# Kernel optimization log

Measured on AMD Instinct MI355X. Metric: run time of the kernel, lower is better.

Reference implementation:

```python
import jax, jax.numpy as jnp
import numpy as np

N = 16384   # total gate nodes (64 graphs x 256 gates)
B = 64      # graphs in batch
E = 49152   # directed edges (avg in-degree 3)
Q = 32      # qubit_num
F = 256     # feat_dim
D = 2 * F   # node feature dim = 512
H = 2       # heads
A = 128     # action_num


def _gatv2(x, wl, wr, att, b, src, dst, n):
    # PyG GATv2Conv (concat=True, share_weights=False, negative_slope=0.2)
    h, c = att.shape
    xl = (x @ wl).reshape(n, h, c)   # source-side projection [N,H,C]
    xr = (x @ wr).reshape(n, h, c)   # target-side projection [N,H,C]
    e = jax.nn.leaky_relu(xl[src] + xr[dst], 0.2)       # [E,H,C]
    logit = jnp.einsum('ehc,hc->eh', e, att)             # [E,H]
    m = jax.ops.segment_max(logit, dst, num_segments=n)  # softmax over in-edges per target
    p = jnp.exp(logit - m[dst])
    den = jax.ops.segment_sum(p, dst, num_segments=n)
    alpha = p / den[dst]                                 # [E,H]
    out = jax.ops.segment_sum(alpha[:, :, None] * xl[src], dst, num_segments=n)
    return out.reshape(n, h * c) + b


def _forward(x, xt_w1, xt_b1, xt_w2, xt_b2,
             g0_wl, g0_wr, g0_att, g0_b,
             g1_wl, g1_wr, g1_att, g1_b,
             g2_wl, g2_wr, g2_att, g2_b,
             g3_wl, g3_wr, g3_att, g3_b,
             g4_wl, g4_wr, g4_att, g4_b,
             ln_w, ln_b, aggr_t,
             m_w1, m_b1, m_w2, m_b2, m_w3, m_b3,
             edge_index, batch):
    lr = lambda v: jax.nn.leaky_relu(v, 0.01)
    # x_trans: Linear -> LeakyReLU -> Linear, then fold qubit-pairs into one node
    h0 = lr(x @ xt_w1 + xt_b1) @ xt_w2 + xt_b2           # [2N, F]
    cx = h0.reshape(-1, D)                               # [N, 2F]
    n = cx.shape[0]
    # GATv2Conv default add_self_loops=True (inputs contain no self loops)
    sl = jnp.arange(n, dtype=edge_index.dtype)
    src = jnp.concatenate([edge_index[0], sl])
    dst = jnp.concatenate([edge_index[1], sl])
    res = cx
    h = lr(_gatv2(cx, g0_wl, g0_wr, g0_att, g0_b, src, dst, n))
    for wl_, wr_, att_, b_ in ((g1_wl, g1_wr, g1_att, g1_b),
                               (g2_wl, g2_wr, g2_att, g2_b),
                               (g3_wl, g3_wr, g3_att, g3_b)):
        h = lr(_gatv2(h, wl_, wr_, att_, b_, src, dst, n))
    h = lr(_gatv2(h, g4_wl, g4_wr, g4_att, g4_b, src, dst, n))
    h = h + res                                           # residual [N, 2F]
    # PyG LayerNorm(mode='graph'): normalize over nodes AND channels per graph
    cnt = jax.ops.segment_sum(jnp.ones((n,), h.dtype), batch, num_segments=B)
    norm = cnt * h.shape[1]
    mean = jax.ops.segment_sum(h.sum(-1), batch, num_segments=B) / norm
    hc = h - mean[batch][:, None]
    var = jax.ops.segment_sum((hc * hc).sum(-1), batch, num_segments=B) / norm
    h = hc / jnp.sqrt(var + 1e-5)[batch][:, None] * ln_w + ln_b
    # SoftmaxAggregation(learn=True): channel-wise softmax over nodes per graph
    logit = h * aggr_t
    mg = jax.ops.segment_max(logit, batch, num_segments=B)
    p = jnp.exp(logit - mg[batch])
    den = jax.ops.segment_sum(p, batch, num_segments=B)
    g = jax.ops.segment_sum((p / den[batch]) * h, batch, num_segments=B)  # [B, 2F]
    # head MLP 512->384->256->128
    o = lr(g @ m_w1 + m_b1)
    o = lr(o @ m_w2 + m_b2)
    return o @ m_w3 + m_b3


def setup_inputs() -> dict:
    key = jax.random.key(0)
    ks = iter(jax.random.split(key, 64))
    def rn(shp, s=0.05):
        return jax.random.normal(next(ks), shp, jnp.float32) * s
    d = {}
    d['x'] = jax.random.normal(next(ks), (2 * N, Q), jnp.float32)
    src = jax.random.randint(next(ks), (E,), 0, N, jnp.int32)
    off = jax.random.randint(next(ks), (E,), 1, N, jnp.int32)
    d['edge_index'] = jnp.stack([src, (src + off) % N])  # no self loops
    d['batch'] = jnp.arange(N, dtype=jnp.int32) // (N // B)
    d['xt_w1'] = rn((Q, F)); d['xt_b1'] = rn((F,))
    d['xt_w2'] = rn((F, F)); d['xt_b2'] = rn((F,))
    d['g0_wl'] = rn((D, H * D)); d['g0_wr'] = rn((D, H * D))
    d['g0_att'] = rn((H, D));    d['g0_b'] = rn((H * D,))
    for i in (1, 2, 3):
        d[f'g{i}_wl'] = rn((H * D, H * D)); d[f'g{i}_wr'] = rn((H * D, H * D))
        d[f'g{i}_att'] = rn((H, D));        d[f'g{i}_b'] = rn((H * D,))
    d['g4_wl'] = rn((H * D, D)); d['g4_wr'] = rn((H * D, D))
    d['g4_att'] = rn((1, D));    d['g4_b'] = rn((D,))
    d['ln_w'] = jnp.ones((D,), jnp.float32); d['ln_b'] = jnp.zeros((D,), jnp.float32)
    d['aggr_t'] = jnp.array(1.0, jnp.float32)
    d['m_w1'] = rn((D, 384)); d['m_b1'] = rn((384,))
    d['m_w2'] = rn((384, 256)); d['m_b2'] = rn((256,))
    d['m_w3'] = rn((256, A)); d['m_b3'] = rn((A,))
    return d


def reference(x, edge_index, batch, xt_w1, xt_b1, xt_w2, xt_b2,
              g0_wl, g0_wr, g0_att, g0_b,
              g1_wl, g1_wr, g1_att, g1_b,
              g2_wl, g2_wr, g2_att, g2_b,
              g3_wl, g3_wr, g3_att, g3_b,
              g4_wl, g4_wr, g4_att, g4_b,
              ln_w, ln_b, aggr_t,
              m_w1, m_b1, m_w2, m_b2, m_w3, m_b3):
    return _forward(x, xt_w1, xt_b1, xt_w2, xt_b2,
                    g0_wl, g0_wr, g0_att, g0_b,
                    g1_wl, g1_wr, g1_att, g1_b,
                    g2_wl, g2_wr, g2_att, g2_b,
                    g3_wl, g3_wr, g3_att, g3_b,
                    g4_wl, g4_wr, g4_att, g4_b,
                    ln_w, ln_b, aggr_t,
                    m_w1, m_b1, m_w2, m_b2, m_w3, m_b3,
                    edge_index, batch)
```

## Files before the change

kernel.cpp:

```cpp
#include <hip/hip_runtime.h>
#include <hip/hip_bf16.h>

typedef __hip_bfloat16 bf16;

#define NN 16384
#define BBG 64
#define EE 49152
#define ET (EE + NN)
#define DD 512
#define NG (NN / BBG)

__device__ __forceinline__ float b2f(bf16 v) { return __bfloat162float(v); }
__device__ __forceinline__ bf16 f2b(float v) { return __float2bfloat16(v); }
__device__ __forceinline__ float sb2f(short s) {
    unsigned u = ((unsigned)(unsigned short)s) << 16;
    return __builtin_bit_cast(float, u);
}
__device__ __forceinline__ short f2bs(float v) {
    bf16 b = f2b(v);
    return __builtin_bit_cast(short, b);
}
__device__ __forceinline__ int clampi(int v, int lo, int hi)
{
    return v < lo ? lo : (v > hi ? hi : v);
}

typedef __attribute__((ext_vector_type(8))) short bf16x8;
typedef __attribute__((ext_vector_type(4))) float f32x4;

#define AS1 __attribute__((address_space(1)))
#define AS3 __attribute__((address_space(3)))

__global__ __launch_bounds__(256) void gemm_mfma_bt(
    const bf16* __restrict__ A, const bf16* __restrict__ Bt,
    const float* __restrict__ bias, float* __restrict__ C,
    bf16* __restrict__ Cb, int M, int N, int K, float slope, int has_act)
{
    __shared__ bf16 As[128 * 32];
    __shared__ bf16 Bs[128 * 32];
    const int tid = threadIdx.x;
    const int w = tid >> 6;
    const int l = tid & 63;
    const int bm = blockIdx.y * 128;
    const int bn = blockIdx.x * 128;
    const int wrow = (w >> 1) * 64;
    const int wcol = (w & 1) * 64;
    const int quad = l >> 4;
    const int c16 = l & 15;

    const int lrow = l >> 2;
    const int lchunk = l & 3;
    const bf16* Ag = A + (size_t)(bm + w * 16 + lrow) * K + lchunk * 8;
    const bf16* Bg = Bt + (size_t)(bn + w * 16 + lrow) * K + lchunk * 8;
    char* AsB = (char*)As;
    char* BsB = (char*)Bs;

    f32x4 acc[4][4] = {};

    for (int k0 = 0; k0 < K; k0 += 32) {
        __builtin_amdgcn_global_load_lds((const AS1 void*)(Ag + k0),
            (AS3 void*)(AsB + w * 1024), 16, 0, 0);
        __builtin_amdgcn_global_load_lds((const AS1 void*)(Ag + (size_t)64 * K + k0),
            (AS3 void*)(AsB + 4096 + w * 1024), 16, 0, 0);
        __builtin_amdgcn_global_load_lds((const AS1 void*)(Bg + k0),
            (AS3 void*)(BsB + w * 1024), 16, 0, 0);
        __builtin_amdgcn_global_load_lds((const AS1 void*)(Bg + (size_t)64 * K + k0),
            (AS3 void*)(BsB + 4096 + w * 1024), 16, 0, 0);
        __syncthreads();

        bf16x8 a[4], b[4];
#pragma unroll
        for (int i = 0; i < 4; i++) {
            int ra = wrow + i * 16 + c16;
            a[i] = *(const bf16x8*)(AsB + ra * 64 + quad * 16);
            int rb = wcol + i * 16 + c16;
            b[i] = *(const bf16x8*)(BsB + rb * 64 + quad * 16);
        }
#pragma unroll
        for (int i = 0; i < 4; i++)
#pragma unroll
            for (int j = 0; j < 4; j++)
                acc[i][j] = __builtin_amdgcn_mfma_f32_16x16x32_bf16(
                    a[i], b[j], acc[i][j], 0, 0, 0);
        __syncthreads();
    }

#pragma unroll
    for (int i = 0; i < 4; i++) {
#pragma unroll
        for (int j = 0; j < 4; j++) {
            int col = bn + wcol + j * 16 + c16;
            float bv = bias ? bias[col] : 0.f;
#pragma unroll
            for (int r = 0; r < 4; r++) {
                int row = bm + wrow + i * 16 + quad * 4 + r;
                float v = acc[i][j][r] + bv;
                if (has_act) v = (v >= 0.f) ? v : v * slope;
                if (C)  C[(size_t)row * N + col] = v;
                if (Cb) Cb[(size_t)row * N + col] = f2b(v);
            }
        }
    }
}

__global__ __launch_bounds__(256) void gemm_mfma_dual(
    const bf16* __restrict__ A, const bf16* __restrict__ Bt,
    bf16* __restrict__ X0, bf16* __restrict__ X1,
    int M, int Ntot, int K, int HC)
{
    __shared__ bf16 As[128 * 32];
    __shared__ bf16 Bs[128 * 32];
    const int tid = threadIdx.x;
    const int w = tid >> 6;
    const int l = tid & 63;
    const int bm = blockIdx.y * 128;
    const int bn = blockIdx.x * 128;
    const int wrow = (w >> 1) * 64;
    const int wcol = (w & 1) * 64;
    const int quad = l >> 4;
    const int c16 = l & 15;

    const int lrow = l >> 2;
    const int lchunk = l & 3;
    const bf16* Ag = A + (size_t)(bm + w * 16 + lrow) * K + lchunk * 8;
    const bf16* Bg = Bt + (size_t)(bn + w * 16 + lrow) * K + lchunk * 8;
    char* AsB = (char*)As;
    char* BsB = (char*)Bs;

    f32x4 acc[4][4] = {};

    for (int k0 = 0; k0 < K; k0 += 32) {
        __builtin_amdgcn_global_load_lds((const AS1 void*)(Ag + k0),
            (AS3 void*)(AsB + w * 1024), 16, 0, 0);
        __builtin_amdgcn_global_load_lds((const AS1 void*)(Ag + (size_t)64 * K + k0),
            (AS3 void*)(AsB + 4096 + w * 1024), 16, 0, 0);
        __builtin_amdgcn_global_load_lds((const AS1 void*)(Bg + k0),
            (AS3 void*)(BsB + w * 1024), 16, 0, 0);
        __builtin_amdgcn_global_load_lds((const AS1 void*)(Bg + (size_t)64 * K + k0),
            (AS3 void*)(BsB + 4096 + w * 1024), 16, 0, 0);
        __syncthreads();

        bf16x8 a[4], b[4];
#pragma unroll
        for (int i = 0; i < 4; i++) {
            int ra = wrow + i * 16 + c16;
            a[i] = *(const bf16x8*)(AsB + ra * 64 + quad * 16);
            int rb = wcol + i * 16 + c16;
            b[i] = *(const bf16x8*)(BsB + rb * 64 + quad * 16);
        }
#pragma unroll
        for (int i = 0; i < 4; i++)
#pragma unroll
            for (int j = 0; j < 4; j++)
                acc[i][j] = __builtin_amdgcn_mfma_f32_16x16x32_bf16(
                    a[i], b[j], acc[i][j], 0, 0, 0);
        __syncthreads();
    }

#pragma unroll
    for (int i = 0; i < 4; i++) {
#pragma unroll
        for (int j = 0; j < 4; j++) {
            int col = bn + wcol + j * 16 + c16;
            bf16* dst = (col < HC) ? (X0 + col) : (X1 + col - HC);
#pragma unroll
            for (int r = 0; r < 4; r++) {
                int row = bm + wrow + i * 16 + quad * 4 + r;
                dst[(size_t)row * HC] = f2b(acc[i][j][r]);
            }
        }
    }
}

__global__ __launch_bounds__(256) void gemm_f32(
    const float* __restrict__ A, const float* __restrict__ W,
    const float* __restrict__ bias, float* __restrict__ C,
    int M, int N, int K, float slope, int has_act)
{
    const int BK = 16;
    __shared__ float Asm[BK][64 + 1];
    __shared__ float Wsm[BK][64 + 1];
    int tid = threadIdx.x;
    int bm = blockIdx.y * 64;
    int bn = blockIdx.x * 64;
    int tr = tid >> 4;
    int tc = tid & 15;
    float acc[4][4] = {};

    for (int k0 = 0; k0 < K; k0 += BK) {
        {
            int col = tid & 15;
            int row = tid >> 4;
#pragma unroll
            for (int p = 0; p < 4; p++) {
                int r = row + p * 16;
                Asm[col][r] = A[(size_t)(bm + r) * K + k0 + col];
            }
        }
        {
            int wc = tid & 63;
            int wr = tid >> 6;
#pragma unroll
            for (int p = 0; p < 4; p++) {
                int r = wr + p * 4;
                Wsm[r][wc] = W[(size_t)(k0 + r) * N + bn + wc];
            }
        }
        __syncthreads();
#pragma unroll
        for (int kk = 0; kk < BK; kk++) {
            float a[4], w[4];
#pragma unroll
            for (int i = 0; i < 4; i++) a[i] = Asm[kk][tr * 4 + i];
#pragma unroll
            for (int j = 0; j < 4; j++) w[j] = Wsm[kk][tc * 4 + j];
#pragma unroll
            for (int i = 0; i < 4; i++)
#pragma unroll
                for (int j = 0; j < 4; j++)
                    acc[i][j] += a[i] * w[j];
        }
        __syncthreads();
    }
#pragma unroll
    for (int i = 0; i < 4; i++) {
        int r = bm + tr * 4 + i;
#pragma unroll
        for (int j = 0; j < 4; j++) {
            int cn = bn + tc * 4 + j;
            float v = acc[i][j];
            if (bias) v += bias[cn];
            if (has_act) v = (v >= 0.f) ? v : v * slope;
            C[(size_t)r * N + cn] = v;
        }
    }
}

__global__ __launch_bounds__(256) void transpose_f2b2(
    const float* __restrict__ in0, bf16* __restrict__ out0,
    const float* __restrict__ in1, bf16* __restrict__ out1, int R, int C)
{
    const float* in = blockIdx.z ? in1 : in0;
    bf16* out = blockIdx.z ? out1 : out0;
    __shared__ float tile[32][33];
    int c0 = blockIdx.x * 32;
    int r0 = blockIdx.y * 32;
    int tx = threadIdx.x & 31;
    int ty = threadIdx.x >> 5;
#pragma unroll
    for (int k = 0; k < 4; k++) {
        int r = ty + k * 8;
        tile[r][tx] = in[(size_t)(r0 + r) * C + c0 + tx];
    }
    __syncthreads();
#pragma unroll
    for (int k = 0; k < 4; k++) {
        int rr = ty + k * 8;
        out[(size_t)(c0 + rr) * R + r0 + tx] = f2b(tile[tx][rr]);
    }
}

__global__ void f2b_vec(const float* __restrict__ in, bf16* __restrict__ out, int n)
{
    int i = blockIdx.x * 256 + threadIdx.x;
    if (i < n) out[i] = f2b(in[i]);
}

__global__ void count_deg(const int* __restrict__ ei, int* __restrict__ deg)
{
    int e = blockIdx.x * 256 + threadIdx.x;
    if (e >= ET) return;
    int d = (e < EE) ? ei[EE + e] : (e - EE);
    d = clampi(d, 0, NN - 1);
    atomicAdd(&deg[d], 1);
}

__global__ __launch_bounds__(256) void scan_deg(const int* __restrict__ deg,
                                                int* __restrict__ rs)
{
    __shared__ int part[256];
    __shared__ int psum[257];
    int tid = threadIdx.x;
    const int per = NN / 256;
    int base = tid * per;
    int s = 0;
    for (int i = 0; i < per; i++) s += deg[base + i];
    part[tid] = s;
    __syncthreads();
    if (tid == 0) {
        int acc = 0;
        for (int i = 0; i < 256; i++) { psum[i] = acc; acc += part[i]; }
        psum[256] = acc;
    }
    __syncthreads();
    int acc = psum[tid];
    for (int i = 0; i < per; i++) { rs[base + i] = acc; acc += deg[base + i]; }
    if (tid == 0) rs[NN] = psum[256];
}

__global__ void fill_csr(const int* __restrict__ ei, const int* __restrict__ rs,
                         int* __restrict__ cur, int* __restrict__ csrc)
{
    int e = blockIdx.x * 256 + threadIdx.x;
    if (e >= ET) return;
    int s, d;
    if (e < EE) { s = ei[e]; d = ei[EE + e]; } else { s = d = e - EE; }
    s = clampi(s, 0, NN - 1);
    d = clampi(d, 0, NN - 1);
    int pos = atomicAdd(&cur[d], 1);
    int slot = clampi(rs[d] + pos, 0, ET - 1);
    csrc[slot] = s;
}

template<int NH>
__global__ __launch_bounds__(256, 4) void gat_wave5(
    const bf16* __restrict__ xl, const bf16* __restrict__ xr,
    const float* __restrict__ att, const float* __restrict__ bias,
    const int* __restrict__ rs, const int* __restrict__ csrc,
    const float* __restrict__ res, float* __restrict__ out_f,
    bf16* __restrict__ out_b, float* __restrict__ lnsums)
{
    constexpr int HC = NH * 512;
    constexpr int PF = 6;
    constexpr int NODES = (NH == 2) ? 8 : 4;
    const int tid = threadIdx.x;
    const int w = tid >> 6;
    const int lane = tid & 63;
    const int wave_id = blockIdx.x * 4 + w;

    int msrc[NODES];
    int sdeg[NODES];
#pragma unroll
    for (int it = 0; it < NODES; ++it) {
        int gw = wave_id * NODES + it;
        int n = (NH == 2) ? (gw >> 1) : gw;
        int st = rs[n];
        int deg = clampi(rs[n + 1] - st, 1, 64);
        st = clampi(st, 0, ET - 1);
        st = __builtin_amdgcn_readfirstlane(st);
        deg = __builtin_amdgcn_readfirstlane(deg);
        sdeg[it] = deg;
        msrc[it] = csrc[st + ((lane < deg) ? lane : deg - 1)];
    }
    if (NH == 2) {
        asm volatile("" : "+v"(msrc[0]), "+v"(msrc[1]), "+v"(msrc[2]),
                          "+v"(msrc[3]), "+v"(msrc[4]), "+v"(msrc[5]),
                          "+v"(msrc[6]), "+v"(msrc[7]));
    } else {
        asm volatile("" : "+v"(msrc[0]), "+v"(msrc[1]), "+v"(msrc[2]),
                          "+v"(msrc[3]));
    }

    float av0[8], av1[8];
    {
        f32x4 t0 = *(const f32x4*)(att + lane * 8);
        f32x4 t1 = *(const f32x4*)(att + lane * 8 + 4);
#pragma unroll
        for (int k = 0; k < 4; k++) { av0[k] = t0[k]; av0[4 + k] = t1[k]; }
        if (NH == 2) {
            f32x4 t2 = *(const f32x4*)(att + 512 + lane * 8);
            f32x4 t3 = *(const f32x4*)(att + 512 + lane * 8 + 4);
#pragma unroll
            for (int k = 0; k < 4; k++) { av1[k] = t2[k]; av1[4 + k] = t3[k]; }
        } else {
#pragma unroll
            for (int k = 0; k < 8; k++) av1[k] = av0[k];
        }
    }

    f32x4 rows[2][PF];
    f32x4 rpx[2];

    auto issue = [&](int it, int pb) {
        int gw = wave_id * NODES + it;
        int n = (NH == 2) ? (gw >> 1) : gw;
        int h = (NH == 2) ? (gw & 1) : 0;
        int cb = h * 512 + lane * 8;
        rpx[pb] = *(const f32x4*)(xr + (size_t)n * HC + cb);
        int dm1 = sdeg[it] - 1;
#pragma unroll
        for (int r = 0; r < PF; r++) {
            int idx = (r < dm1) ? r : dm1;
            int s = __builtin_amdgcn_readlane(msrc[it], idx);
            s = clampi(s, 0, NN - 1);
            rows[pb][r] = *(const f32x4*)(xl + (size_t)s * HC + cb);
        }
    };
    auto pin = [&](int pb) {
        asm volatile("" : "+v"(rows[pb][0]), "+v"(rows[pb][1]),
                          "+v"(rows[pb][2]), "+v"(rows[pb][3]),
                          "+v"(rows[pb][4]), "+v"(rows[pb][5]), "+v"(rpx[pb]));
    };

    auto compute = [&](int it, int pb) {
        int gw = wave_id * NODES + it;
        int n = (NH == 2) ? (gw >> 1) : gw;
        int h = (NH == 2) ? (gw & 1) : 0;
        int cb = h * 512 + lane * 8;
        int deg = sdeg[it];

        float rv[8], av[8];
        {
            bf16x8 xb = __builtin_bit_cast(bf16x8, rpx[pb]);
#pragma unroll
            for (int k = 0; k < 8; k++) {
                rv[k] = sb2f(xb[k]);
                av[k] = h ? av1[k] : av0[k];
            }
        }

        float part[PF];
#pragma unroll
        for (int r = 0; r < PF; r++) {
            bf16x8 rb = __builtin_bit_cast(bf16x8, rows[pb][r]);
            float p0 = 0.f, p1 = 0.f, p2 = 0.f, p3 = 0.f;
#pragma unroll
            for (int k = 0; k < 8; k += 4) {
                float x0 = sb2f(rb[k + 0]);
                float x1 = sb2f(rb[k + 1]);
                float x2 = sb2f(rb[k + 2]);
                float x3 = sb2f(rb[k + 3]);
                float u0 = x0 + rv[k + 0]; u0 = (u0 >= 0.f) ? u0 : 0.2f * u0;
                float u1 = x1 + rv[k + 1]; u1 = (u1 >= 0.f) ? u1 : 0.2f * u1;
                float u2 = x2 + rv[k + 2]; u2 = (u2 >= 0.f) ? u2 : 0.2f * u2;
                float u3 = x3 + rv[k + 3]; u3 = (u3 >= 0.f) ? u3 : 0.2f * u3;
                p0 = fmaf(av[k + 0], u0, p0);
                p1 = fmaf(av[k + 1], u1, p1);
                p2 = fmaf(av[k + 2], u2, p2);
                p3 = fmaf(av[k + 3], u3, p3);
            }
            part[r] = (p0 + p1) + (p2 + p3);
        }

#pragma unroll
        for (int msk = 32; msk; msk >>= 1) {
#pragma unroll
            for (int r = 0; r < PF; r++) part[r] += __shfl_xor(part[r], msk);
        }

        float m = -1e30f;
#pragma unroll
        for (int r = 0; r < PF; r++) {
            float vr = (r < deg) ? part[r] : -1e30f;
            m = fmaxf(m, vr);
        }
        float den = 0.f;
        float pw[PF];
#pragma unroll
        for (int r = 0; r < PF; r++) {
            float e = __expf(part[r] - m);
            pw[r] = (r < deg) ? e : 0.f;
            den += pw[r];
        }

        float acc[8];
#pragma unroll
        for (int k = 0; k < 8; k++) acc[k] = 0.f;
#pragma unroll
        for (int r = 0; r < PF; r++) {
            bf16x8 rb = __builtin_bit_cast(bf16x8, rows[pb][r]);
#pragma unroll
            for (int k = 0; k < 8; k++)
                acc[k] = fmaf(pw[r], sb2f(rb[k]), acc[k]);
        }

        if (deg > PF) {
            for (int i = PF; i < deg; i++) {
                int s = __builtin_amdgcn_readlane(msrc[it], i);
                s = clampi(s, 0, NN - 1);
                f32x4 rw = *(const f32x4*)(xl + (size_t)s * HC + cb);
                bf16x8 rb = __builtin_bit_cast(bf16x8, rw);
                float pt = 0.f;
#pragma unroll
                for (int k = 0; k < 8; k++) {
                    float x = sb2f(rb[k]);
                    float u = x + rv[k];
                    u = (u >= 0.f) ? u : 0.2f * u;
                    pt = fmaf(av[k], u, pt);
                }
#pragma unroll
                for (int msk = 32; msk; msk >>= 1) pt += __shfl_xor(pt, msk);
                float mn = fmaxf(m, pt);
                float rr = __expf(m - mn);
                float pi = __expf(pt - mn);
                m = mn;
                den = den * rr + pi;
#pragma unroll
                for (int k = 0; k < 8; k++) {
                    float x = sb2f(rb[k]);
                    acc[k] = fmaf(acc[k], rr, pi * x);
                }
            }
        }

        float inv = 1.f / den;
        f32x4 b0 = *(const f32x4*)(bias + cb);
        f32x4 b1 = *(const f32x4*)(bias + cb + 4);
        float vals[8];
#pragma unroll
        for (int k = 0; k < 8; k++) {
            float bv = (k < 4) ? b0[k] : b1[k - 4];
            float v = fmaf(acc[k], inv, bv);
            v = (v >= 0.f) ? v : 0.01f * v;
            vals[k] = v;
        }
        if (res) {
            float ls = 0.f, ls2 = 0.f;
#pragma unroll
            for (int k = 0; k < 8; k++) {
                vals[k] += res[(size_t)n * HC + cb + k];
                ls += vals[k];
                ls2 += vals[k] * vals[k];
            }
#pragma unroll
            for (int v = 0; v < 2; v++) {
                f32x4 ov;
#pragma unroll
                for (int k = 0; k < 4; k++) ov[k] = vals[v * 4 + k];
                *(f32x4*)(out_f + (size_t)n * HC + cb + v * 4) = ov;
            }
            if (lnsums) {
#pragma unroll
                for (int msk = 32; msk; msk >>= 1) {
                    ls += __shfl_xor(ls, msk);
                    ls2 += __shfl_xor(ls2, msk);
                }
                if (lane == 0) {
                    int g = n >> 8;
                    atomicAdd(&lnsums[g], ls);
                    atomicAdd(&lnsums[BBG + g], ls2);
                }
            }
        } else {
            bf16x8 ov;
#pragma unroll
            for (int k = 0; k < 8; k++) ov[k] = f2bs(vals[k]);
            *(bf16x8*)(out_b + (size_t)n * HC + cb) = ov;
        }
    };

    issue(0, 0);
    pin(0);
#pragma unroll
    for (int it = 0; it < NODES; ++it) {
        int pb = it & 1;
        if (it + 1 < NODES) {
            issue(it + 1, pb ^ 1);
            pin(pb ^ 1);
        }
        compute(it, pb);
    }
}

__global__ __launch_bounds__(256) void aggr_partial(
    const float* __restrict__ h, const float* __restrict__ lnsums,
    const float* __restrict__ lnw, const float* __restrict__ lnb,
    const float* __restrict__ t_, float* __restrict__ pm,
    float* __restrict__ pd, float* __restrict__ pa)
{
    int g = blockIdx.x, ch = blockIdx.y, nk = blockIdx.z;
    int tid = threadIdx.x;
    int c = ch * 256 + tid;
    const float tot = (float)(NG * DD);
    float S = lnsums[g], S2 = lnsums[BBG + g];
    float mu = S / tot;
    float iv = rsqrtf(fmaxf(S2 / tot - mu * mu, 0.f) + 1e-5f);
    float w = lnw[c], b = lnb[c], t = t_[0];
    size_t base = (size_t)g * NG * DD + (size_t)nk * 32 * DD + c;
    float m = -1e30f, den = 0.f, acc = 0.f;
    for (int i = 0; i < 32; i++) {
        float hn = (h[base + (size_t)i * DD] - mu) * iv * w + b;
        float lg = hn * t;
        if (lg > m) {
            float r = __expf(m - lg);
            den *= r; acc *= r; m = lg;
        }
        float p = __expf(lg - m);
        den += p; acc += p * hn;
    }
    size_t idx = (((size_t)g * 2 + ch) * 8 + nk) * 256 + tid;
    pm[idx] = m; pd[idx] = den; pa[idx] = acc;
}

__global__ __launch_bounds__(256) void aggr_combine(
    const float* __restrict__ pm, const float* __restrict__ pd,
    const float* __restrict__ pa, float* __restrict__ gout)
{
    int g = blockIdx.x, ch = blockIdx.y;
    int tid = threadIdx.x;
    size_t base = (((size_t)g * 2 + ch) * 8) * 256 + tid;
    float m = -1e30f;
#pragma unroll
    for (int k = 0; k < 8; k++) m = fmaxf(m, pm[base + k * 256]);
    float den = 0.f, acc = 0.f;
#pragma unroll
    for (int k = 0; k < 8; k++) {
        float r = __expf(pm[base + k * 256] - m);
        den += pd[base + k * 256] * r;
        acc += pa[base + k * 256] * r;
    }
    gout[(size_t)g * DD + ch * 256 + tid] = acc / den;
}

extern "C" void kernel_launch(void* const* d_in, const int* in_sizes, int n_in,
                              void* d_out, int out_size, void* d_ws, size_t ws_size,
                              hipStream_t stream)
{
    const float* x      = (const float*)d_in[0];
    const int*   ei     = (const int*)d_in[1];
    const float* xt_w1  = (const float*)d_in[3];
    const float* xt_b1  = (const float*)d_in[4];
    const float* xt_w2  = (const float*)d_in[5];
    const float* xt_b2  = (const float*)d_in[6];
    const float* ln_w   = (const float*)d_in[27];
    const float* ln_b   = (const float*)d_in[28];
    const float* aggr_t = (const float*)d_in[29];
    const float* m_w1   = (const float*)d_in[30];
    const float* m_b1   = (const float*)d_in[31];
    const float* m_w2   = (const float*)d_in[32];
    const float* m_b2   = (const float*)d_in[33];
    const float* m_w3   = (const float*)d_in[34];
    const float* m_b3   = (const float*)d_in[35];
    float* out = (float*)d_out;

    char* p = (char*)d_ws;
    auto take = [&](size_t bytes) {
        char* r = p;
        p += (bytes + 255) & ~(size_t)255;
        return r;
    };
    int* i_deg     = (int*)take((size_t)(NN + 1) * 4);
    int* i_rs      = (int*)take((size_t)(NN + 1) * 4);
    int* i_cur     = (int*)take((size_t)NN * 4);
    int* i_src     = (int*)take((size_t)ET * 4);
    float* f_sums  = (float*)take((size_t)2 * BBG * 4);
    float* f_pm    = (float*)take((size_t)BBG * 2 * 8 * 256 * 4);
    float* f_pd    = (float*)take((size_t)BBG * 2 * 8 * 256 * 4);
    float* f_pa    = (float*)take((size_t)BBG * 2 * 8 * 256 * 4);
    float* b_g     = (float*)take((size_t)BBG * DD * 4);
    float* b_m1    = (float*)take((size_t)BBG * 384 * 4);
    float* b_m2    = (float*)take((size_t)BBG * 256 * 4);
    float* b_res   = (float*)take((size_t)NN * DD * 4);
    float* b_h     = (float*)take((size_t)NN * DD * 4);
    bf16* b_resb   = (bf16*)take((size_t)NN * DD * 2);
    bf16* b_hb     = (bf16*)take((size_t)NN * 1024 * 2);
    bf16* b_xlb    = (bf16*)take((size_t)NN * 1024 * 2);
    bf16* b_xrb    = (bf16*)take((size_t)NN * 1024 * 2);
    bf16* b_xb     = (bf16*)take((size_t)2 * NN * 32 * 2);
    bf16* b_wcat   = (bf16*)take((size_t)2048 * 1024 * 2);
    bf16* b_w1b    = (bf16*)take((size_t)32 * 256 * 2);
    bf16* b_w2b    = (bf16*)take((size_t)256 * 256 * 2);
    bf16* b_t1b = b_hb;

    dim3 blk(256);

    hipMemsetAsync(i_deg, 0, (size_t)(NN + 1) * 4, stream);
    hipMemsetAsync(i_cur, 0, (size_t)NN * 4, stream);
    hipMemsetAsync(f_sums, 0, (size_t)2 * BBG * 4, stream);
    count_deg<<<ET / 256, blk, 0, stream>>>(ei, i_deg);
    scan_deg<<<1, blk, 0, stream>>>(i_deg, i_rs);
    fill_csr<<<ET / 256, blk, 0, stream>>>(ei, i_rs, i_cur, i_src);

    f2b_vec<<<(2 * NN * 32 + 255) / 256, blk, 0, stream>>>(x, b_xb, 2 * NN * 32);
    transpose_f2b2<<<dim3(256 / 32, 32 / 32, 1), blk, 0, stream>>>(
        xt_w1, b_w1b, xt_w1, b_w1b, 32, 256);
    transpose_f2b2<<<dim3(256 / 32, 256 / 32, 1), blk, 0, stream>>>(
        xt_w2, b_w2b, xt_w2, b_w2b, 256, 256);

    gemm_mfma_bt<<<dim3(256 / 128, 32768 / 128), blk, 0, stream>>>(
        b_xb, b_w1b, xt_b1, (float*)nullptr, b_t1b, 32768, 256, 32, 0.01f, 1);
    gemm_mfma_bt<<<dim3(256 / 128, 32768 / 128), blk, 0, stream>>>(
        b_t1b, b_w2b, xt_b2, b_res, b_resb, 32768, 256, 256, 0.f, 0);

    for (int L = 0; L < 5; L++) {
        const float* wl  = (const float*)d_in[7 + 4 * L];
        const float* wr  = (const float*)d_in[8 + 4 * L];
        const float* att = (const float*)d_in[9 + 4 * L];
        const float* gb  = (const float*)d_in[10 + 4 * L];
        int Fin = (L == 0) ? 512 : 1024;
        int HC  = (L == 4) ? 512 : 1024;
        const bf16* hin = (L == 0) ? b_resb : b_hb;

        transpose_f2b2<<<dim3(HC / 32, Fin / 32, 2), blk, 0, stream>>>(
            wl, b_wcat, wr, b_wcat + (size_t)HC * Fin, Fin, HC);
        gemm_mfma_dual<<<dim3(2 * HC / 128, NN / 128), blk, 0, stream>>>(
            hin, b_wcat, b_xlb, b_xrb, NN, 2 * HC, Fin, HC);
        if (L == 4) {
            gat_wave5<1><<<1024, blk, 0, stream>>>(
                b_xlb, b_xrb, att, gb, i_rs, i_src,
                b_res, b_h, (bf16*)nullptr, f_sums);
        } else {
            gat_wave5<2><<<1024, blk, 0, stream>>>(
                b_xlb, b_xrb, att, gb, i_rs, i_src,
                (const float*)nullptr, (float*)nullptr, b_hb, (float*)nullptr);
        }
    }

    aggr_partial<<<dim3(BBG, 2, 8), blk, 0, stream>>>(
        b_h, f_sums, ln_w, ln_b, aggr_t, f_pm, f_pd, f_pa);
    aggr_combine<<<dim3(BBG, 2), blk, 0, stream>>>(f_pm, f_pd, f_pa, b_g);

    gemm_f32<<<dim3(384 / 64, 1), blk, 0, stream>>>(
        b_g, m_w1, m_b1, b_m1, 64, 384, 512, 0.01f, 1);
    gemm_f32<<<dim3(256 / 64, 1), blk, 0, stream>>>(
        b_m1, m_w2, m_b2, b_m2, 64, 256, 384, 0.01f, 1);
    gemm_f32<<<dim3(128 / 64, 1), blk, 0, stream>>>(
        b_m2, m_w3, m_b3, out, 64, 128, 256, 0.f, 0);
}
```

Baseline: 1.116 ms.

## Stage GAT gathered rows through LDS via async global_load_lds double buffering

The GAT aggregation kernel now gathers neighbor xl rows, the xr row and (for the last layer) the residual row straight into LDS with global_load_lds. It double-buffers them per wave with explicit vmcnt waits, replacing the register-pinned prefetch. Bias is preloaded into registers once, and the last layer launches with 128-thread blocks. The aim is to cut VGPR pressure and raise occupancy while keeping loads in flight. The cost is LDS usage, extra LDS reads, and reliance on hand-counted vmcnt values matching the issued loads.

```diff
diff --git a/kernel.cpp b/kernel.cpp
--- a/kernel.cpp
+++ b/kernel.cpp
@@ -313,7 +313,7 @@
 }
 
 template<int NH>
-__global__ __launch_bounds__(256, 4) void gat_wave5(
+__global__ __launch_bounds__(256) void gat_wave7(
     const bf16* __restrict__ xl, const bf16* __restrict__ xr,
     const float* __restrict__ att, const float* __restrict__ bias,
     const int* __restrict__ rs, const int* __restrict__ csrc,
@@ -323,10 +323,14 @@
     constexpr int HC = NH * 512;
     constexpr int PF = 6;
     constexpr int NODES = (NH == 2) ? 8 : 4;
+    constexpr int WPB = (NH == 2) ? 4 : 2;
+    constexpr int SLOTS = (NH == 2) ? 7 : 9;
+    __shared__ char smem[WPB * 2 * SLOTS * 1024];
+
     const int tid = threadIdx.x;
     const int w = tid >> 6;
     const int lane = tid & 63;
-    const int wave_id = blockIdx.x * 4 + w;
+    const int wave_id = blockIdx.x * WPB + w;
 
     int msrc[NODES];
     int sdeg[NODES];
@@ -342,54 +346,59 @@
         sdeg[it] = deg;
         msrc[it] = csrc[st + ((lane < deg) ? lane : deg - 1)];
     }
-    if (NH == 2) {
-        asm volatile("" : "+v"(msrc[0]), "+v"(msrc[1]), "+v"(msrc[2]),
-                          "+v"(msrc[3]), "+v"(msrc[4]), "+v"(msrc[5]),
-                          "+v"(msrc[6]), "+v"(msrc[7]));
-    } else {
-        asm volatile("" : "+v"(msrc[0]), "+v"(msrc[1]), "+v"(msrc[2]),
-                          "+v"(msrc[3]));
-    }
-
-    float av0[8], av1[8];
+
+    float av0[8], av1[8], bv0[8], bv1[8];
     {
         f32x4 t0 = *(const f32x4*)(att + lane * 8);
         f32x4 t1 = *(const f32x4*)(att + lane * 8 + 4);
-#pragma unroll
-        for (int k = 0; k < 4; k++) { av0[k] = t0[k]; av0[4 + k] = t1[k]; }
+        f32x4 u0 = *(const f32x4*)(bias + lane * 8);
+        f32x4 u1 = *(const f32x4*)(bias + lane * 8 + 4);
+#pragma unroll
+        for (int k = 0; k < 4; k++) {
+            av0[k] = t0[k]; av0[4 + k] = t1[k];
+            bv0[k] = u0[k]; bv0[4 + k] = u1[k];
+        }
         if (NH == 2) {
             f32x4 t2 = *(const f32x4*)(att + 512 + lane * 8);
             f32x4 t3 = *(const f32x4*)(att + 512 + lane * 8 + 4);
-#pragma unroll
-            for (int k = 0; k < 4; k++) { av1[k] = t2[k]; av1[4 + k] = t3[k]; }
+            f32x4 u2 = *(const f32x4*)(bias + 512 + lane * 8);
+            f32x4 u3 = *(const f32x4*)(bias + 512 + lane * 8 + 4);
+#pragma unroll
+            for (int k = 0; k < 4; k++) {
+                av1[k] = t2[k]; av1[4 + k] = t3[k];
+                bv1[k] = u2[k]; bv1[4 + k] = u3[k];
+            }
         } else {
 #pragma unroll
-            for (int k = 0; k < 8; k++) av1[k] = av0[k];
-        }
-    }
-
-    f32x4 rows[2][PF];
-    f32x4 rpx[2];
+            for (int k = 0; k < 8; k++) { av1[k] = av0[k]; bv1[k] = bv0[k]; }
+        }
+    }
 
     auto issue = [&](int it, int pb) {
         int gw = wave_id * NODES + it;
         int n = (NH == 2) ? (gw >> 1) : gw;
         int h = (NH == 2) ? (gw & 1) : 0;
-        int cb = h * 512 + lane * 8;
-        rpx[pb] = *(const f32x4*)(xr + (size_t)n * HC + cb);
+        char* buf = smem + (size_t)((w * 2 + pb) * SLOTS) * 1024;
+        const bf16* xrrow = xr + (size_t)n * HC + h * 512 + lane * 8;
+        __builtin_amdgcn_global_load_lds((const AS1 void*)xrrow,
+            (AS3 void*)buf, 16, 0, 0);
         int dm1 = sdeg[it] - 1;
 #pragma unroll
         for (int r = 0; r < PF; r++) {
             int idx = (r < dm1) ? r : dm1;
             int s = __builtin_amdgcn_readlane(msrc[it], idx);
             s = clampi(s, 0, NN - 1);
-            rows[pb][r] = *(const f32x4*)(xl + (size_t)s * HC + cb);
-        }
-    };
-    auto pin = [&](int pb) {
-        asm volatile("" : "+v"(rows[pb][0]), "+v"(rows[pb][1]),
-                          "+v"(rows[pb][2]), "+v"(rows[pb][3]),
-                          "+v"(rows[pb][4]), "+v"(rows[pb][5]), "+v"(rpx[pb]));
+            const bf16* row = xl + (size_t)s * HC + h * 512 + lane * 8;
+            __builtin_amdgcn_global_load_lds((const AS1 void*)row,
+                (AS3 void*)(buf + (1 + r) * 1024), 16, 0, 0);
+        }
+        if (NH == 1) {
+            const float* rr = res + (size_t)n * 512 + lane * 4;
+            __builtin_amdgcn_global_load_lds((const AS1 void*)rr,
+                (AS3 void*)(buf + 7 * 1024), 16, 0, 0);
+            __builtin_amdgcn_global_load_lds((const AS1 void*)(rr + 256),
+                (AS3 void*)(buf + 8 * 1024), 16, 0, 0);
+        }
     };
 
     auto compute = [&](int it, int pb) {
@@ -398,28 +407,32 @@
         int h = (NH == 2) ? (gw & 1) : 0;
         int cb = h * 512 + lane * 8;
         int deg = sdeg[it];
+        char* buf = smem + (size_t)((w * 2 + pb) * SLOTS) * 1024;
 
         float rv[8], av[8];
         {
-            bf16x8 xb = __builtin_bit_cast(bf16x8, rpx[pb]);
+            bf16x8 xb = *(const bf16x8*)(buf + lane * 16);
 #pragma unroll
             for (int k = 0; k < 8; k++) {
                 rv[k] = sb2f(xb[k]);
                 av[k] = h ? av1[k] : av0[k];
             }
         }
+        bf16x8 rloc[PF];
+#pragma unroll
+        for (int r = 0; r < PF; r++)
+            rloc[r] = *(const bf16x8*)(buf + (1 + r) * 1024 + lane * 16);
 
         float part[PF];
 #pragma unroll
         for (int r = 0; r < PF; r++) {
-            bf16x8 rb = __builtin_bit_cast(bf16x8, rows[pb][r]);
             float p0 = 0.f, p1 = 0.f, p2 = 0.f, p3 = 0.f;
 #pragma unroll
             for (int k = 0; k < 8; k += 4) {
-                float x0 = sb2f(rb[k + 0]);
-                float x1 = sb2f(rb[k + 1]);
-                float x2 = sb2f(rb[k + 2]);
-                float x3 = sb2f(rb[k + 3]);
+                float x0 = sb2f(rloc[r][k + 0]);
+                float x1 = sb2f(rloc[r][k + 1]);
+                float x2 = sb2f(rloc[r][k + 2]);
+                float x3 = sb2f(rloc[r][k + 3]);
                 float u0 = x0 + rv[k + 0]; u0 = (u0 >= 0.f) ? u0 : 0.2f * u0;
                 float u1 = x1 + rv[k + 1]; u1 = (u1 >= 0.f) ? u1 : 0.2f * u1;
                 float u2 = x2 + rv[k + 2]; u2 = (u2 >= 0.f) ? u2 : 0.2f * u2;
@@ -458,10 +471,9 @@
         for (int k = 0; k < 8; k++) acc[k] = 0.f;
 #pragma unroll
         for (int r = 0; r < PF; r++) {
-            bf16x8 rb = __builtin_bit_cast(bf16x8, rows[pb][r]);
 #pragma unroll
             for (int k = 0; k < 8; k++)
-                acc[k] = fmaf(pw[r], sb2f(rb[k]), acc[k]);
+                acc[k] = fmaf(pw[r], sb2f(rloc[r][k]), acc[k]);
         }
 
         if (deg > PF) {
@@ -494,21 +506,21 @@
         }
 
         float inv = 1.f / den;
-        f32x4 b0 = *(const f32x4*)(bias + cb);
-        f32x4 b1 = *(const f32x4*)(bias + cb + 4);
         float vals[8];
 #pragma unroll
         for (int k = 0; k < 8; k++) {
-            float bv = (k < 4) ? b0[k] : b1[k - 4];
+            float bv = h ? bv1[k] : bv0[k];
             float v = fmaf(acc[k], inv, bv);
             v = (v >= 0.f) ? v : 0.01f * v;
             vals[k] = v;
         }
-        if (res) {
+        if (NH == 1) {
+            f32x4 r0 = *(const f32x4*)(buf + 7 * 1024 + lane * 32);
+            f32x4 r1 = *(const f32x4*)(buf + 7 * 1024 + lane * 32 + 16);
             float ls = 0.f, ls2 = 0.f;
 #pragma unroll
             for (int k = 0; k < 8; k++) {
-                vals[k] += res[(size_t)n * HC + cb + k];
+                vals[k] += (k < 4) ? r0[k] : r1[k - 4];
                 ls += vals[k];
                 ls2 += vals[k] * vals[k];
             }
@@ -519,17 +531,15 @@
                 for (int k = 0; k < 4; k++) ov[k] = vals[v * 4 + k];
                 *(f32x4*)(out_f + (size_t)n * HC + cb + v * 4) = ov;
             }
-            if (lnsums) {
-#pragma unroll
-                for (int msk = 32; msk; msk >>= 1) {
-                    ls += __shfl_xor(ls, msk);
-                    ls2 += __shfl_xor(ls2, msk);
-                }
-                if (lane == 0) {
-                    int g = n >> 8;
-                    atomicAdd(&lnsums[g], ls);
-                    atomicAdd(&lnsums[BBG + g], ls2);
-                }
+#pragma unroll
+            for (int msk = 32; msk; msk >>= 1) {
+                ls += __shfl_xor(ls, msk);
+                ls2 += __shfl_xor(ls2, msk);
+            }
+            if (lane == 0) {
+                int g = n >> 8;
+                atomicAdd(&lnsums[g], ls);
+                atomicAdd(&lnsums[BBG + g], ls2);
             }
         } else {
             bf16x8 ov;
@@ -540,14 +550,17 @@
     };
 
     issue(0, 0);
-    pin(0);
 #pragma unroll
     for (int it = 0; it < NODES; ++it) {
         int pb = it & 1;
         if (it + 1 < NODES) {
             issue(it + 1, pb ^ 1);
-            pin(pb ^ 1);
-        }
+            if (NH == 2) asm volatile("s_waitcnt vmcnt(7)" ::: "memory");
+            else         asm volatile("s_waitcnt vmcnt(9)" ::: "memory");
+        } else {
+            asm volatile("s_waitcnt vmcnt(0)" ::: "memory");
+        }
+        __builtin_amdgcn_sched_barrier(0);
         compute(it, pb);
     }
 }
@@ -686,11 +699,11 @@
         gemm_mfma_dual<<<dim3(2 * HC / 128, NN / 128), blk, 0, stream>>>(
             hin, b_wcat, b_xlb, b_xrb, NN, 2 * HC, Fin, HC);
         if (L == 4) {
-            gat_wave5<1><<<1024, blk, 0, stream>>>(
+            gat_wave7<1><<<2048, dim3(128), 0, stream>>>(
                 b_xlb, b_xrb, att, gb, i_rs, i_src,
                 b_res, b_h, (bf16*)nullptr, f_sums);
         } else {
-            gat_wave5<2><<<1024, blk, 0, stream>>>(
+            gat_wave7<2><<<1024, blk, 0, stream>>>(
                 b_xlb, b_xrb, att, gb, i_rs, i_src,
                 (const float*)nullptr, (float*)nullptr, b_hb, (float*)nullptr);
         }
```

After: 1.048 ms. 6.1% less time.
